# Optimization experiments

Hardware: AMD Instinct MI355X
Metric: run time of the kernel (lower is better)

The kernel has to match this reference:

```python
import jax, jax.numpy as jnp
import numpy as np

B, T, E, D, H, DK, DV, C, FILT = 32, 2048, 1024, 1024, 4, 512, 512, 10, 100
K = 2 * FILT + 1  # conv kernel width = 201
SCALING = 2.0     # default forward scaling arg


def setup_inputs() -> dict:
    key = jax.random.key(0)
    ks = jax.random.split(key, 12)
    s = 0.02
    enc_hs_pad = jax.random.normal(ks[0], (B, T, E), dtype=jnp.float32)
    enc_hs_len = jax.random.randint(ks[1], (B,), T // 2, T + 1).astype(jnp.int32)
    dec_z = jax.random.normal(ks[2], (B, D), dtype=jnp.float32)
    # default att_prev in the module: uniform over valid frames (per head)
    valid = (jnp.arange(T)[None, :] < enc_hs_len[:, None]).astype(jnp.float32)  # (B,T)
    att_prev = jnp.broadcast_to((valid / enc_hs_len[:, None].astype(jnp.float32))[:, None, :], (B, H, T))
    return {
        "enc_hs_pad": enc_hs_pad,
        "enc_hs_len": enc_hs_len,
        "dec_z": dec_z,
        "att_prev": att_prev,
        "Wq": s * jax.random.normal(ks[3], (H, D, DK), dtype=jnp.float32),
        "bq": s * jax.random.normal(ks[4], (H, DK), dtype=jnp.float32),
        "Wk": s * jax.random.normal(ks[5], (H, E, DK), dtype=jnp.float32),
        "Wv": s * jax.random.normal(ks[6], (H, E, DV), dtype=jnp.float32),
        "gw": s * jax.random.normal(ks[7], (H, DK), dtype=jnp.float32),
        "gb": s * jax.random.normal(ks[8], (H,), dtype=jnp.float32),
        "conv_w": s * jax.random.normal(ks[9], (H, C, K), dtype=jnp.float32),
        "Watt": s * jax.random.normal(ks[10], (H, C, DK), dtype=jnp.float32),
        "Wo": s * jax.random.normal(ks[11], (H * DV, E), dtype=jnp.float32),
    }


def reference(enc_hs_pad, enc_hs_len, dec_z, att_prev, Wq, bq, Wk, Wv, gw, gb, conv_w, Watt, Wo):
    b, t, _ = enc_hs_pad.shape
    h, c_ch, kw = conv_w.shape
    # per-head key/value precomputes (vectorized over heads)
    k = jnp.einsum('bte,hek->bhtk', enc_hs_pad, Wk)          # (B,H,T,DK)
    v = jnp.einsum('bte,hev->bhtv', enc_hs_pad, Wv)          # (B,H,T,DV)
    q = jnp.einsum('bd,hdk->bhk', dec_z, Wq) + bq[None]      # (B,H,DK)
    # location conv: grouped 1D conv over T, one group per head
    conv_out = jax.lax.conv_general_dilated(
        att_prev,                                   # (B, H, T)
        conv_w.reshape(h * c_ch, 1, kw),            # (H*C, 1, K)
        window_strides=(1,),
        padding=[(FILT, FILT)],
        feature_group_count=h,
        dimension_numbers=('NCH', 'OIH', 'NCH'),
    ).reshape(b, h, c_ch, t)                        # (B,H,C,T)
    loc = jnp.einsum('bhct,hck->bhtk', conv_out, Watt)       # (B,H,T,DK)
    # additive score: gvec(tanh(k + loc + q))
    e = jnp.einsum('bhtk,hk->bht', jnp.tanh(k + loc + q[:, :, None, :]), gw) + gb[None, :, None]
    pad_mask = jnp.arange(t)[None, :] >= enc_hs_len[:, None]  # (B,T) True at pads
    e = jnp.where(pad_mask[:, None, :], -jnp.inf, e)
    w = jax.nn.softmax(SCALING * e, axis=-1)                 # (B,H,T)
    c = jnp.einsum('bhtv,bht->bhv', v, w).reshape(b, h * v.shape[-1]) @ Wo  # (B,E)
    return c, w
```

## Files before the change

kernel.cpp:

```cpp
#include <hip/hip_runtime.h>
#include <math.h>

#define B_ 32
#define T_ 2048
#define E_ 1024
#define D_ 1024
#define H_ 4
#define DK_ 512
#define DV_ 512
#define C_ 10
#define FILT_ 100
#define KW_ 201
#define SCALING_ 2.0f
#define KEXT_ 32

typedef __bf16 bf16_t;
typedef __bf16 bf16x8 __attribute__((ext_vector_type(8)));
typedef float f32x4 __attribute__((ext_vector_type(4)));

__device__ __forceinline__ float fast_tanh(float x) {
    x = fminf(15.f, fmaxf(-15.f, x));
    float e = __expf(2.f * x);
    return (e - 1.f) / (e + 1.f);
}

__device__ __forceinline__ void gload16(const void* g, void* l) {
  __builtin_amdgcn_global_load_lds(
      (const __attribute__((address_space(1))) void*)g,
      (__attribute__((address_space(3))) void*)l, 16, 0, 0);
}

__global__ __launch_bounds__(256) void tobf16_kernel(
    const float* __restrict__ in, bf16_t* __restrict__ out) {
  size_t i = ((size_t)blockIdx.x * 256 + threadIdx.x) * 8;
  float4 a = *(const float4*)(in + i);
  float4 b = *(const float4*)(in + i + 4);
  bf16x8 o;
  o[0] = (bf16_t)a.x; o[1] = (bf16_t)a.y; o[2] = (bf16_t)a.z; o[3] = (bf16_t)a.w;
  o[4] = (bf16_t)b.x; o[5] = (bf16_t)b.y; o[6] = (bf16_t)b.z; o[7] = (bf16_t)b.w;
  *(bf16x8*)(out + i) = o;
}

__global__ __launch_bounds__(256) void wkt_kernel(
    const float* __restrict__ Wk, bf16_t* __restrict__ WkT) {
  __shared__ float t[32][33];
  int h = blockIdx.z;
  int dk0 = blockIdx.x * 32, e0 = blockIdx.y * 32;
  int x = threadIdx.x & 31, y0 = threadIdx.x >> 5;
  for (int yy = 0; yy < 32; yy += 8) {
    int y = y0 + yy;
    t[y][x] = Wk[((size_t)h * E_ + e0 + y) * DK_ + dk0 + x];
  }
  __syncthreads();
  for (int yy = 0; yy < 32; yy += 8) {
    int y = y0 + yy;
    WkT[((size_t)h * DK_ + dk0 + y) * E_ + e0 + x] = (bf16_t)t[x][y];
  }
}

#define QSPLIT 8
__global__ __launch_bounds__(256) void qproj_kernel(
    const float* __restrict__ dec_z, const float* __restrict__ Wq,
    const float* __restrict__ bq, float* __restrict__ q) {
  int idx = blockIdx.x * 256 + threadIdx.x;
  int s = blockIdx.y;
  int dk = idx & (DK_ - 1);
  int h  = (idx >> 9) & (H_ - 1);
  int b  = idx >> 11;
  const int CH = D_ / QSPLIT;
  const float* dz = dec_z + (size_t)b * D_ + s * CH;
  const float* w  = Wq + (size_t)h * D_ * DK_ + (size_t)(s * CH) * DK_ + dk;
  float acc = (s == 0) ? bq[h * DK_ + dk] : 0.f;
  for (int d = 0; d < CH; ++d) acc += dz[d] * w[(size_t)d * DK_];
  atomicAdd(q + idx, acc);
}

__global__ __launch_bounds__(256) void cwt_kernel(
    const float* __restrict__ cw, float* __restrict__ cwT) {
  int idx = blockIdx.x * 256 + threadIdx.x;
  if (idx < H_ * C_ * KW_) {
    int k = idx % KW_;
    int c = (idx / KW_) % C_;
    int h = idx / (KW_ * C_);
    cwT[((size_t)h * KW_ + k) * C_ + c] = cw[idx];
  }
}

__global__ __launch_bounds__(256) void conv_kernel(
    const float* __restrict__ att_prev, const float* __restrict__ cwT,
    bf16_t* __restrict__ convT) {
  int bh = blockIdx.y;
  int h  = bh & (H_ - 1);
  int t0 = blockIdx.x * 256;
  int tid = threadIdx.x;
  __shared__ float sh[256 + 2 * FILT_];
  const float* ap = att_prev + (size_t)bh * T_;
  for (int f = tid; f < 256 + 2 * FILT_; f += 256) {
    int t = t0 + f - FILT_;
    sh[f] = (t >= 0 && t < T_) ? ap[t] : 0.f;
  }
  __syncthreads();
  const float* wt = cwT + (size_t)h * KW_ * C_;
  float out[C_];
#pragma unroll
  for (int c = 0; c < C_; ++c) out[c] = 0.f;
  for (int k = 0; k < KW_; ++k) {
    float x = sh[tid + k];
    const float* wk = wt + k * C_;
#pragma unroll
    for (int c = 0; c < C_; ++c) out[c] += wk[c] * x;
  }
  bf16_t* o = convT + ((size_t)bh * T_ + t0 + tid) * KEXT_;
#pragma unroll
  for (int c = 0; c < C_; ++c) o[c] = (bf16_t)out[c];
  o[C_] = (bf16_t)1.0f;
#pragma unroll
  for (int c = C_ + 1; c < KEXT_; ++c) o[c] = (bf16_t)0.0f;
}

__global__ __launch_bounds__(256) void bext_kernel(
    const float* __restrict__ Watt, const float* __restrict__ q,
    bf16_t* __restrict__ Bext) {
  int idx = blockIdx.x * 256 + threadIdx.x;
  int dk = idx & (DK_ - 1);
  int h = (idx >> 9) & (H_ - 1);
  bf16_t* o = Bext + (size_t)idx * KEXT_;
#pragma unroll
  for (int c = 0; c < C_; ++c) o[c] = (bf16_t)Watt[((size_t)h * C_ + c) * DK_ + dk];
  o[C_] = (bf16_t)q[idx];
#pragma unroll
  for (int c = C_ + 1; c < KEXT_; ++c) o[c] = (bf16_t)0.0f;
}

#define WT 128
#define WN 128
#define WKB 64
__global__ __launch_bounds__(256) void e_mfma_kernel(
    const bf16_t* __restrict__ encb, const bf16_t* __restrict__ WkT,
    const bf16_t* __restrict__ convT, const bf16_t* __restrict__ Bext,
    const float* __restrict__ gw, float* __restrict__ e_out) {
  __shared__ bf16_t As[WT * WKB];
  __shared__ bf16_t Bs[WN * WKB];
  int tid = threadIdx.x;
  int wave = tid >> 6, lane = tid & 63;
  int bh = blockIdx.z;
  int b = bh >> 2, h = bh & 3;
  int t0 = blockIdx.y * WT;
  int n0b = blockIdx.x * WN;
  const bf16_t* Ag = encb + ((size_t)b * T_ + t0) * E_;
  const bf16_t* Bg = WkT + ((size_t)h * DK_ + n0b) * E_;

  f32x4 acc[4][4] = {};

  int m0 = (wave & 1) * 64, n0 = (wave >> 1) * 64;
  int lr = lane & 15, lk = (lane >> 4) * 8;
  int srow = wave * 32 + (lane >> 3);
  int cb   = lane & 7;

  for (int e0 = 0; e0 < E_; e0 += WKB) {
#pragma unroll
    for (int j = 0; j < 4; ++j) {
      int r = srow + j * 8;
      int gc = (cb ^ (r & 7)) * 8;
      gload16(Ag + (size_t)r * E_ + e0 + gc, As + r * WKB + cb * 8);
      gload16(Bg + (size_t)r * E_ + e0 + gc, Bs + r * WKB + cb * 8);
    }
    __syncthreads();
#pragma unroll
    for (int kk = 0; kk < WKB; kk += 32) {
      int sc = ((((kk + lk) >> 3) ^ (lr & 7)) << 3);
      bf16x8 af[4], bfv[4];
#pragma unroll
      for (int i = 0; i < 4; ++i) {
        af[i]  = *(const bf16x8*)(As + (m0 + i * 16 + lr) * WKB + sc);
        bfv[i] = *(const bf16x8*)(Bs + (n0 + i * 16 + lr) * WKB + sc);
      }
#pragma unroll
      for (int i = 0; i < 4; ++i)
#pragma unroll
        for (int j = 0; j < 4; ++j)
          acc[i][j] = __builtin_amdgcn_mfma_f32_16x16x32_bf16(
              af[i], bfv[j], acc[i][j], 0, 0, 0);
    }
    __syncthreads();
  }

  {
    const bf16_t* Ag2 = convT + ((size_t)bh * T_ + t0) * KEXT_;
    const bf16_t* Bg2 = Bext + ((size_t)bh * DK_ + n0b) * KEXT_;
    int srow2 = wave * 32 + (lane >> 2);
    int scol2 = (lane & 3) * 8;
#pragma unroll
    for (int j = 0; j < 2; ++j) {
      int r = srow2 + j * 16;
      gload16(Ag2 + (size_t)r * KEXT_ + scol2, As + r * KEXT_ + scol2);
      gload16(Bg2 + (size_t)r * KEXT_ + scol2, Bs + r * KEXT_ + scol2);
    }
    __syncthreads();
    bf16x8 af[4], bfv[4];
#pragma unroll
    for (int i = 0; i < 4; ++i) {
      af[i]  = *(const bf16x8*)(As + (m0 + i * 16 + lr) * KEXT_ + lk);
      bfv[i] = *(const bf16x8*)(Bs + (n0 + i * 16 + lr) * KEXT_ + lk);
    }
#pragma unroll
    for (int i = 0; i < 4; ++i)
#pragma unroll
      for (int j = 0; j < 4; ++j)
        acc[i][j] = __builtin_amdgcn_mfma_f32_16x16x32_bf16(
            af[i], bfv[j], acc[i][j], 0, 0, 0);
  }

  float gwv[4];
#pragma unroll
  for (int j = 0; j < 4; ++j)
    gwv[j] = gw[(size_t)h * DK_ + n0b + n0 + j * 16 + lr];
  int rquad = (lane >> 4) * 4;
#pragma unroll
  for (int i = 0; i < 4; ++i) {
#pragma unroll
    for (int r = 0; r < 4; ++r) {
      int row = m0 + i * 16 + rquad + r;
      float part = 0.f;
#pragma unroll
      for (int j = 0; j < 4; ++j)
        part += fast_tanh(acc[i][j][r]) * gwv[j];
#pragma unroll
      for (int off = 8; off > 0; off >>= 1) part += __shfl_xor(part, off, 64);
      if (lr == 0) atomicAdd(e_out + (size_t)bh * T_ + t0 + row, part);
    }
  }
}

__global__ __launch_bounds__(256) void softmax_kernel(
    const float* __restrict__ e, const float* __restrict__ gb,
    const int* __restrict__ len, float* __restrict__ w_out) {
  int bh = blockIdx.x;
  int b = bh >> 2, h = bh & 3;
  int tid = threadIdx.x;
  int L = len[b];
  const float* er = e + (size_t)bh * T_;
  float* wr = w_out + (size_t)bh * T_;
  float gbh = gb[h];
  __shared__ float redA[4], redB[4];
  float mx = -1e30f;
  for (int t = tid; t < T_; t += 256)
    if (t < L) mx = fmaxf(mx, er[t] + gbh);
#pragma unroll
  for (int off = 32; off > 0; off >>= 1) mx = fmaxf(mx, __shfl_xor(mx, off, 64));
  if ((tid & 63) == 0) redA[tid >> 6] = mx;
  __syncthreads();
  mx = fmaxf(fmaxf(redA[0], redA[1]), fmaxf(redA[2], redA[3]));
  float sum = 0.f;
  for (int t = tid; t < T_; t += 256)
    if (t < L) sum += __expf(SCALING_ * ((er[t] + gbh) - mx));
#pragma unroll
  for (int off = 32; off > 0; off >>= 1) sum += __shfl_xor(sum, off, 64);
  if ((tid & 63) == 0) redB[tid >> 6] = sum;
  __syncthreads();
  sum = redB[0] + redB[1] + redB[2] + redB[3];
  float inv = 1.f / sum;
  for (int t = tid; t < T_; t += 256)
    wr[t] = (t < L) ? __expf(SCALING_ * ((er[t] + gbh) - mx)) * inv : 0.f;
}

#define TCH 256
__global__ __launch_bounds__(256) void wenc_kernel(
    const float* __restrict__ enc, const float* __restrict__ w,
    const int* __restrict__ len, float* __restrict__ we) {
  int b = blockIdx.y;
  int t0 = blockIdx.x * TCH;
  int L = len[b];
  if (t0 >= L) return;
  int tid = threadIdx.x;
  __shared__ float wS[H_ * TCH];
  const float* wb = w + (size_t)b * H_ * T_;
#pragma unroll
  for (int l = 0; l < H_; ++l)
    wS[l * TCH + tid] = wb[(size_t)l * T_ + t0 + tid];
  __syncthreads();
  const float4* encb = (const float4*)(enc + (size_t)b * T_ * E_);
  int tmax = min(TCH, L - t0);
  float4 a0 = {0.f, 0.f, 0.f, 0.f}, a1 = a0, a2 = a0, a3 = a0;
  for (int tt = 0; tt < tmax; ++tt) {
    float4 x = encb[(size_t)(t0 + tt) * (E_ / 4) + tid];
    float w0 = wS[tt], w1 = wS[TCH + tt], w2 = wS[2 * TCH + tt], w3 = wS[3 * TCH + tt];
    a0.x += w0 * x.x; a0.y += w0 * x.y; a0.z += w0 * x.z; a0.w += w0 * x.w;
    a1.x += w1 * x.x; a1.y += w1 * x.y; a1.z += w1 * x.z; a1.w += w1 * x.w;
    a2.x += w2 * x.x; a2.y += w2 * x.y; a2.z += w2 * x.z; a2.w += w2 * x.w;
    a3.x += w3 * x.x; a3.y += w3 * x.y; a3.z += w3 * x.z; a3.w += w3 * x.w;
  }
  float* p = we + (size_t)b * H_ * E_ + tid * 4;
  atomicAdd(p + 0 * E_ + 0, a0.x); atomicAdd(p + 0 * E_ + 1, a0.y);
  atomicAdd(p + 0 * E_ + 2, a0.z); atomicAdd(p + 0 * E_ + 3, a0.w);
  atomicAdd(p + 1 * E_ + 0, a1.x); atomicAdd(p + 1 * E_ + 1, a1.y);
  atomicAdd(p + 1 * E_ + 2, a1.z); atomicAdd(p + 1 * E_ + 3, a1.w);
  atomicAdd(p + 2 * E_ + 0, a2.x); atomicAdd(p + 2 * E_ + 1, a2.y);
  atomicAdd(p + 2 * E_ + 2, a2.z); atomicAdd(p + 2 * E_ + 3, a2.w);
  atomicAdd(p + 3 * E_ + 0, a3.x); atomicAdd(p + 3 * E_ + 1, a3.y);
  atomicAdd(p + 3 * E_ + 2, a3.z); atomicAdd(p + 3 * E_ + 3, a3.w);
}

#define CSPLIT 8
__global__ __launch_bounds__(256) void ctx_kernel(
    const float* __restrict__ we, const float* __restrict__ Wv,
    float* __restrict__ ctx) {
  int idx = blockIdx.x * 256 + threadIdx.x;
  int s = blockIdx.y;
  int dv = idx & (DV_ - 1);
  int bh = idx >> 9;
  int h = bh & 3;
  const int CH = E_ / CSPLIT;
  const float* weh = we + (size_t)bh * E_ + s * CH;
  const float* wvp = Wv + (size_t)h * E_ * DV_ + (size_t)(s * CH) * DV_ + dv;
  float acc = 0.f;
  for (int e = 0; e < CH; ++e) acc += weh[e] * wvp[(size_t)e * DV_];
  atomicAdd(ctx + idx, acc);
}

#define OSPLIT 8
__global__ __launch_bounds__(256) void out_kernel(
    const float* __restrict__ ctx, const float* __restrict__ Wo,
    float* __restrict__ c_out) {
  int eo = blockIdx.x * 256 + threadIdx.x;
  int b = blockIdx.y;
  int s = blockIdx.z;
  const int CH = (H_ * DV_) / OSPLIT;
  const float* cb = ctx + (size_t)b * (H_ * DV_) + s * CH;
  const float* wp = Wo + (size_t)(s * CH) * E_ + eo;
  float acc = 0.f;
  for (int i = 0; i < CH; ++i) acc += cb[i] * wp[(size_t)i * E_];
  atomicAdd(c_out + (size_t)b * E_ + eo, acc);
}

extern "C" void kernel_launch(void* const* d_in, const int* in_sizes, int n_in,
                              void* d_out, int out_size, void* d_ws, size_t ws_size,
                              hipStream_t stream) {
  const float* enc  = (const float*)d_in[0];
  const int*   len  = (const int*)d_in[1];
  const float* decz = (const float*)d_in[2];
  const float* attp = (const float*)d_in[3];
  const float* Wq   = (const float*)d_in[4];
  const float* bq   = (const float*)d_in[5];
  const float* Wk   = (const float*)d_in[6];
  const float* Wv   = (const float*)d_in[7];
  const float* gw   = (const float*)d_in[8];
  const float* gb   = (const float*)d_in[9];
  const float* cw   = (const float*)d_in[10];
  const float* Watt = (const float*)d_in[11];
  const float* Wo   = (const float*)d_in[12];

  float* c_out = (float*)d_out;
  float* w_out = c_out + (size_t)B_ * E_;

  float* q    = (float*)d_ws;
  float* e    = q   + (size_t)B_ * H_ * DK_;
  float* we   = e   + (size_t)B_ * H_ * T_;
  float* ctx  = we  + (size_t)B_ * H_ * E_;
  float* cwT  = ctx + (size_t)B_ * H_ * DV_;
  bf16_t* encb16 = (bf16_t*)(cwT + (size_t)H_ * KW_ * C_ + 64);
  bf16_t* WkT    = encb16 + (size_t)B_ * T_ * E_;
  bf16_t* convT  = WkT + (size_t)H_ * DK_ * E_;
  bf16_t* Bext   = convT + (size_t)B_ * H_ * T_ * KEXT_;

  hipMemsetAsync(q, 0, (size_t)B_ * H_ * DK_ * sizeof(float), stream);
  hipMemsetAsync(e, 0, (size_t)B_ * H_ * T_ * sizeof(float), stream);
  hipMemsetAsync(we, 0, (size_t)B_ * H_ * E_ * sizeof(float), stream);
  hipMemsetAsync(ctx, 0, (size_t)B_ * H_ * DV_ * sizeof(float), stream);
  hipMemsetAsync(c_out, 0, (size_t)B_ * E_ * sizeof(float), stream);

  tobf16_kernel<<<(size_t)B_ * T_ * E_ / 8 / 256, 256, 0, stream>>>(enc, encb16);
  wkt_kernel<<<dim3(DK_ / 32, E_ / 32, H_), 256, 0, stream>>>(Wk, WkT);
  qproj_kernel<<<dim3(B_ * H_ * DK_ / 256, QSPLIT), 256, 0, stream>>>(decz, Wq, bq, q);
  cwt_kernel<<<(H_ * C_ * KW_ + 255) / 256, 256, 0, stream>>>(cw, cwT);
  conv_kernel<<<dim3(T_ / 256, B_ * H_), 256, 0, stream>>>(attp, cwT, convT);
  bext_kernel<<<B_ * H_ * DK_ / 256, 256, 0, stream>>>(Watt, q, Bext);
  e_mfma_kernel<<<dim3(DK_ / WN, T_ / WT, B_ * H_), 256, 0, stream>>>(
      encb16, WkT, convT, Bext, gw, e);
  softmax_kernel<<<B_ * H_, 256, 0, stream>>>(e, gb, len, w_out);
  wenc_kernel<<<dim3(T_ / TCH, B_), 256, 0, stream>>>(enc, w_out, len, we);
  ctx_kernel<<<dim3(B_ * H_ * DV_ / 256, CSPLIT), 256, 0, stream>>>(we, Wv, ctx);
  out_kernel<<<dim3(E_ / 256, B_, OSPLIT), 256, 0, stream>>>(ctx, Wo, c_out);
}
```

Before: 1.108 ms.

## Deepen e_mfma K-tile, reorder grid for head locality, use bf16 encoder in wenc

Doubles the K-step of the score GEMM tile to 128, with a 16-way XOR swizzle and a flat load mapping. This halves the number of barrier iterations but doubles LDS use per block. The grid is remapped so that all heads and DK tiles for one batch and time tile sit next to each other, so the shared encoder tile is more likely to be reused from L2. The weighted-encoder reduction now reads the bf16 copy instead of fp32, halving its memory traffic at some precision cost. The four workspace memsets are merged into one.

```diff
diff --git a/kernel.cpp b/kernel.cpp
--- a/kernel.cpp
+++ b/kernel.cpp
@@ -15,6 +15,7 @@
 #define KEXT_ 32
 
 typedef __bf16 bf16_t;
+typedef __bf16 bf16x4 __attribute__((ext_vector_type(4)));
 typedef __bf16 bf16x8 __attribute__((ext_vector_type(8)));
 typedef float f32x4 __attribute__((ext_vector_type(4)));
 
@@ -134,7 +135,7 @@
 
 #define WT 128
 #define WN 128
-#define WKB 64
+#define WKB 128
 __global__ __launch_bounds__(256) void e_mfma_kernel(
     const bf16_t* __restrict__ encb, const bf16_t* __restrict__ WkT,
     const bf16_t* __restrict__ convT, const bf16_t* __restrict__ Bext,
@@ -143,10 +144,11 @@
   __shared__ bf16_t Bs[WN * WKB];
   int tid = threadIdx.x;
   int wave = tid >> 6, lane = tid & 63;
-  int bh = blockIdx.z;
-  int b = bh >> 2, h = bh & 3;
+  int xdk = blockIdx.x & 3, h = blockIdx.x >> 2;
+  int b = blockIdx.z;
+  int bh = b * H_ + h;
   int t0 = blockIdx.y * WT;
-  int n0b = blockIdx.x * WN;
+  int n0b = xdk * WN;
   const bf16_t* Ag = encb + ((size_t)b * T_ + t0) * E_;
   const bf16_t* Bg = WkT + ((size_t)h * DK_ + n0b) * E_;
 
@@ -154,21 +156,21 @@
 
   int m0 = (wave & 1) * 64, n0 = (wave >> 1) * 64;
   int lr = lane & 15, lk = (lane >> 4) * 8;
-  int srow = wave * 32 + (lane >> 3);
-  int cb   = lane & 7;
 
   for (int e0 = 0; e0 < E_; e0 += WKB) {
 #pragma unroll
-    for (int j = 0; j < 4; ++j) {
-      int r = srow + j * 8;
-      int gc = (cb ^ (r & 7)) * 8;
-      gload16(Ag + (size_t)r * E_ + e0 + gc, As + r * WKB + cb * 8);
-      gload16(Bg + (size_t)r * E_ + e0 + gc, Bs + r * WKB + cb * 8);
+    for (int j = 0; j < 8; ++j) {
+      int s = tid + 256 * j;
+      int r = s >> 4, cbk = s & 15;
+      int gc = (cbk ^ (r & 15)) * 8;
+      gload16(Ag + (size_t)r * E_ + e0 + gc, As + r * WKB + cbk * 8);
+      gload16(Bg + (size_t)r * E_ + e0 + gc, Bs + r * WKB + cbk * 8);
     }
     __syncthreads();
 #pragma unroll
     for (int kk = 0; kk < WKB; kk += 32) {
-      int sc = ((((kk + lk) >> 3) ^ (lr & 7)) << 3);
+      int CB = (kk + lk) >> 3;
+      int sc = (CB ^ lr) << 3;
       bf16x8 af[4], bfv[4];
 #pragma unroll
       for (int i = 0; i < 4; ++i) {
@@ -266,7 +268,7 @@
 
 #define TCH 256
 __global__ __launch_bounds__(256) void wenc_kernel(
-    const float* __restrict__ enc, const float* __restrict__ w,
+    const bf16_t* __restrict__ encb, const float* __restrict__ w,
     const int* __restrict__ len, float* __restrict__ we) {
   int b = blockIdx.y;
   int t0 = blockIdx.x * TCH;
@@ -279,11 +281,12 @@
   for (int l = 0; l < H_; ++l)
     wS[l * TCH + tid] = wb[(size_t)l * T_ + t0 + tid];
   __syncthreads();
-  const float4* encb = (const float4*)(enc + (size_t)b * T_ * E_);
+  const bf16_t* eb = encb + (size_t)b * T_ * E_;
   int tmax = min(TCH, L - t0);
   float4 a0 = {0.f, 0.f, 0.f, 0.f}, a1 = a0, a2 = a0, a3 = a0;
   for (int tt = 0; tt < tmax; ++tt) {
-    float4 x = encb[(size_t)(t0 + tt) * (E_ / 4) + tid];
+    bf16x4 xb = *(const bf16x4*)(eb + (size_t)(t0 + tt) * E_ + tid * 4);
+    float4 x = {(float)xb[0], (float)xb[1], (float)xb[2], (float)xb[3]};
     float w0 = wS[tt], w1 = wS[TCH + tt], w2 = wS[2 * TCH + tt], w3 = wS[3 * TCH + tt];
     a0.x += w0 * x.x; a0.y += w0 * x.y; a0.z += w0 * x.z; a0.w += w0 * x.w;
     a1.x += w1 * x.x; a1.y += w1 * x.y; a1.z += w1 * x.z; a1.w += w1 * x.w;
@@ -363,10 +366,8 @@
   bf16_t* convT  = WkT + (size_t)H_ * DK_ * E_;
   bf16_t* Bext   = convT + (size_t)B_ * H_ * T_ * KEXT_;
 
-  hipMemsetAsync(q, 0, (size_t)B_ * H_ * DK_ * sizeof(float), stream);
-  hipMemsetAsync(e, 0, (size_t)B_ * H_ * T_ * sizeof(float), stream);
-  hipMemsetAsync(we, 0, (size_t)B_ * H_ * E_ * sizeof(float), stream);
-  hipMemsetAsync(ctx, 0, (size_t)B_ * H_ * DV_ * sizeof(float), stream);
+  size_t zero_floats = (size_t)B_ * H_ * (DK_ + T_ + E_ + DV_);
+  hipMemsetAsync(q, 0, zero_floats * sizeof(float), stream);
   hipMemsetAsync(c_out, 0, (size_t)B_ * E_ * sizeof(float), stream);
 
   tobf16_kernel<<<(size_t)B_ * T_ * E_ / 8 / 256, 256, 0, stream>>>(enc, encb16);
@@ -375,10 +376,10 @@
   cwt_kernel<<<(H_ * C_ * KW_ + 255) / 256, 256, 0, stream>>>(cw, cwT);
   conv_kernel<<<dim3(T_ / 256, B_ * H_), 256, 0, stream>>>(attp, cwT, convT);
   bext_kernel<<<B_ * H_ * DK_ / 256, 256, 0, stream>>>(Watt, q, Bext);
-  e_mfma_kernel<<<dim3(DK_ / WN, T_ / WT, B_ * H_), 256, 0, stream>>>(
+  e_mfma_kernel<<<dim3((DK_ / WN) * H_, T_ / WT, B_), 256, 0, stream>>>(
       encb16, WkT, convT, Bext, gw, e);
   softmax_kernel<<<B_ * H_, 256, 0, stream>>>(e, gb, len, w_out);
-  wenc_kernel<<<dim3(T_ / TCH, B_), 256, 0, stream>>>(enc, w_out, len, we);
+  wenc_kernel<<<dim3(T_ / TCH, B_), 256, 0, stream>>>(encb16, w_out, len, we);
   ctx_kernel<<<dim3(B_ * H_ * DV_ / 256, CSPLIT), 256, 0, stream>>>(we, Wv, ctx);
   out_kernel<<<dim3(E_ / 256, B_, OSPLIT), 256, 0, stream>>>(ctx, Wo, c_out);
 }
```

Result: faster. 994.9 us (-10.2%).
